# Kernel tuning notes

Hardware: AMD Instinct MI355X
Metric: run time of the kernel (lower is better)

The kernel has to match this reference:

```python
import jax, jax.numpy as jnp
import numpy as np

B, QL, DL, H = 16, 1024, 4096, 128


def setup_inputs() -> dict:
    key = jax.random.key(0)
    k1, k2, k3, k4, k5 = jax.random.split(key, 5)
    return {
        "query_input": jax.random.normal(k1, (B, QL, H), dtype=jnp.float32),
        "query_mask": jax.random.randint(k2, (B, QL), 0, 2, dtype=jnp.int32),
        "doc_input": jax.random.normal(k3, (B, DL, H), dtype=jnp.float32),
        "doc_mask": jax.random.randint(k4, (B, DL), 0, 2, dtype=jnp.int32),
        "sim_matrix": jax.random.normal(k5, (B, QL, DL), dtype=jnp.float32),
    }


def reference(query_input, query_mask, doc_input, doc_mask, sim_matrix):
    # query_input: (b, q, d); doc_input: (b, k, d); sim_matrix: (b, q, k)
    dim = query_input.shape[-1]
    scale = 1.0 / jnp.sqrt(jnp.asarray(dim, dtype=query_input.dtype))
    scores = jnp.einsum("bqd,bkd->bqk", query_input, doc_input) * scale
    # mask out padded doc positions (broadcast doc_mask over query axis)
    scores = jnp.where(doc_mask[:, None, :] == 0, jnp.asarray(-9999.0, scores.dtype), scores)
    attn = jax.nn.softmax(scores, axis=-1)  # (b, q, k)
    # sim-weighted reduction over doc axis, then sum over query axis
    query_atten_sim = jnp.sum(attn * sim_matrix, axis=-1)  # (b, q)
    return jnp.sum(query_atten_sim, axis=-1, keepdims=True)  # (b, 1)
```

## Files before the change

### kernel.cpp

```cpp
#include <hip/hip_runtime.h>
#include <hip/hip_bf16.h>

#define NB 16
#define QL 1024
#define DLEN 4096
#define HD 128

#define KCB 128
#define NKC (DLEN / KCB)
#define NIT (QL / 16)
#define SIMPAN (16 * KCB * 4)
#define QPAN (16 * HD * 4)

typedef __attribute__((ext_vector_type(8))) short short8;
typedef __attribute__((ext_vector_type(4))) float f32x4;

__device__ __forceinline__ short bf16_of(float x) {
  union { __hip_bfloat16 h; short s; } u;
  u.h = __float2bfloat16(x);
  return u.s;
}

__device__ __forceinline__ short8 cvt8(float4 a, float4 b) {
  short8 r;
  r[0] = bf16_of(a.x); r[1] = bf16_of(a.y); r[2] = bf16_of(a.z); r[3] = bf16_of(a.w);
  r[4] = bf16_of(b.x); r[5] = bf16_of(b.y); r[6] = bf16_of(b.z); r[7] = bf16_of(b.w);
  return r;
}

__global__ __launch_bounds__(256, 2) void atten_cross(
    const float* __restrict__ qin, const float* __restrict__ doc,
    const int* __restrict__ dmask, const float* __restrict__ sim,
    float2* __restrict__ ws) {
  const int flat = blockIdx.x;
  const int b = flat & 15;
  const int kc = flat >> 4;
  const int tid = threadIdx.x;
  const int w = tid >> 6;
  const int lane = tid & 63;
  const int grp = lane >> 4;
  const int li = lane & 15;
  const int k0 = kc * KCB + w * 32;

  __shared__ char simbuf[3 * SIMPAN];
  __shared__ char qbuf[3 * QPAN];

  const float* dsrc = doc + ((size_t)b * DLEN + k0 + li) * HD + grp * 8;
  short8 afr[2][4];
#pragma unroll
  for (int kt = 0; kt < 2; ++kt)
#pragma unroll
    for (int cc = 0; cc < 4; ++cc) {
      const float* p = dsrc + (size_t)kt * 16 * HD + cc * 32;
      afr[kt][cc] = cvt8(*(const float4*)p, *(const float4*)(p + 4));
    }
  const int* mp = dmask + (size_t)b * DLEN + k0 + grp * 4;
  const int4 mk0 = *(const int4*)(mp);
  const int4 mk1 = *(const int4*)(mp + 16);

  const char* gsim = (const char*)sim + ((size_t)b * QL) * (DLEN * 4) + (size_t)kc * (KCB * 4);
  const char* gq = (const char*)qin + ((size_t)b * QL) * (HD * 4);
  const char* ssrc[2];
  const char* qsrc[2];
  int sdd[2];
#pragma unroll
  for (int j = 0; j < 2; ++j) {
    const int dd = w * 2048 + j * 1024 + lane * 16;
    const int row = dd >> 9, o = dd & 511;
    const int osw = o ^ ((row & 7) << 4);
    ssrc[j] = gsim + (size_t)row * (DLEN * 4) + osw;
    qsrc[j] = gq + (size_t)row * (HD * 4) + osw;
    sdd[j] = dd;
  }

#define STAGE(it, pan)                                                         \
  {                                                                            \
    const size_t so = (size_t)(it) * (16 * DLEN * 4);                          \
    const size_t qo = (size_t)(it) * (16 * HD * 4);                            \
    _Pragma("unroll") for (int j = 0; j < 2; ++j)                              \
      __builtin_amdgcn_global_load_lds(                                        \
          (const __attribute__((address_space(1))) void*)(ssrc[j] + so),       \
          (__attribute__((address_space(3))) void*)(simbuf + (pan)*SIMPAN + sdd[j]), \
          16, 0, 0);                                                           \
    _Pragma("unroll") for (int j = 0; j < 2; ++j)                              \
      __builtin_amdgcn_global_load_lds(                                        \
          (const __attribute__((address_space(1))) void*)(qsrc[j] + qo),       \
          (__attribute__((address_space(3))) void*)(qbuf + (pan)*QPAN + sdd[j]), \
          16, 0, 0);                                                           \
  }

  constexpr float scale = 0.088388347648318447f;
  const int qxor = (li & 7) << 4;
  const int mm0[4] = {mk0.x, mk0.y, mk0.z, mk0.w};
  const int mm1[4] = {mk1.x, mk1.y, mk1.z, mk1.w};

  STAGE(0, 0);
  STAGE(1, 1);

#pragma unroll 1
  for (int it = 0; it < NIT; ++it) {
    if (it == 0)      asm volatile("s_waitcnt vmcnt(4)" ::: "memory");
    else if (it == 1) asm volatile("s_waitcnt vmcnt(5)" ::: "memory");
    else              asm volatile("s_waitcnt vmcnt(6)" ::: "memory");
    __builtin_amdgcn_s_barrier();
    asm volatile("" ::: "memory");

    {
      const int nx = (it + 2 < NIT) ? it + 2 : NIT - 1;
      STAGE(nx, (it + 2) % 3);
    }

    const char* sp = simbuf + (it % 3) * SIMPAN;
    const char* qp = qbuf + (it % 3) * QPAN;

    short8 bfrag[4];
#pragma unroll
    for (int cc = 0; cc < 4; ++cc) {
      const int o0 = grp * 32 + cc * 128;
      const float4 a = *(const float4*)(qp + li * 512 + (o0 ^ qxor));
      const float4 bb = *(const float4*)(qp + li * 512 + ((o0 + 16) ^ qxor));
      bfrag[cc] = cvt8(a, bb);
    }

    float l = 0.f, nn = 0.f;
#pragma unroll
    for (int kt = 0; kt < 2; ++kt) {
      f32x4 acc = {0.f, 0.f, 0.f, 0.f};
      acc = __builtin_amdgcn_mfma_f32_16x16x32_bf16(afr[kt][0], bfrag[0], acc, 0, 0, 0);
      acc = __builtin_amdgcn_mfma_f32_16x16x32_bf16(afr[kt][1], bfrag[1], acc, 0, 0, 0);
      acc = __builtin_amdgcn_mfma_f32_16x16x32_bf16(afr[kt][2], bfrag[2], acc, 0, 0, 0);
      acc = __builtin_amdgcn_mfma_f32_16x16x32_bf16(afr[kt][3], bfrag[3], acc, 0, 0, 0);
      const int so_ = w * 128 + kt * 64 + grp * 16;
      const f32x4 sv = *(const f32x4*)(sp + li * 512 + (so_ ^ qxor));
#pragma unroll
      for (int r = 0; r < 4; ++r) {
        float e = __expf(acc[r] * scale);
        e = (kt ? mm1[r] : mm0[r]) ? e : 0.f;
        l += e;
        nn = fmaf(e, sv[r], nn);
      }
    }

    l += __shfl_xor(l, 16, 64); l += __shfl_xor(l, 32, 64);
    nn += __shfl_xor(nn, 16, 64); nn += __shfl_xor(nn, 32, 64);
    if (lane < 16) {
      ws[((size_t)(kc * 4 + w) * NB + b) * QL + it * 16 + li] = make_float2(l, nn);
    }
  }
#undef STAGE
}

__global__ __launch_bounds__(1024) void finish(const float2* __restrict__ ws,
                                               float* __restrict__ out) {
  const int b = blockIdx.x;
  const int q = threadIdx.x;
  float l = 0.f, n = 0.f;
#pragma unroll 4
  for (int s = 0; s < NKC * 4; ++s) {
    const float2 v = ws[((size_t)s * NB + b) * QL + q];
    l += v.x;
    n += v.y;
  }
  float v = n / l;
#pragma unroll
  for (int m = 1; m <= 32; m <<= 1) v += __shfl_xor(v, m, 64);
  __shared__ float red[16];
  const int wid = threadIdx.x >> 6, lane = threadIdx.x & 63;
  if (lane == 0) red[wid] = v;
  __syncthreads();
  if (threadIdx.x < 64) {
    float t = (threadIdx.x < 16) ? red[threadIdx.x] : 0.f;
#pragma unroll
    for (int m = 1; m <= 8; m <<= 1) t += __shfl_xor(t, m, 64);
    if (threadIdx.x == 0) out[b] = t;
  }
}

extern "C" void kernel_launch(void* const* d_in, const int* in_sizes, int n_in,
                              void* d_out, int out_size, void* d_ws, size_t ws_size,
                              hipStream_t stream) {
  const float* qin = (const float*)d_in[0];
  const float* doc = (const float*)d_in[2];
  const int* dmask = (const int*)d_in[3];
  const float* sim = (const float*)d_in[4];
  float* out = (float*)d_out;
  float2* ws = (float2*)d_ws;

  dim3 grid(NB * NKC);
  atten_cross<<<grid, 256, 0, stream>>>(qin, doc, dmask, sim, ws);
  finish<<<NB, 1024, 0, stream>>>(ws, out);
}
```

Before: 111.5 us.

## Pre-convert queries to bf16 in a separate pass and double the q-tile per iteration

Adds a small pre-pass kernel that converts the fp32 query tensor to bf16 once, into workspace. The main kernel then stages half-size bf16 query panels straight into LDS, with no per-block re-conversion. It also processes 32 query rows per pipeline step instead of 16, which halves the barrier/iteration count and enlarges the sim and query LDS panels (wait counts adjusted). The cost is an extra launch plus a bf16 write and read of the queries, and higher LDS use that could reduce occupancy.

Measured after the change: 104.0 us. -6.8%, faster.

```diff
diff --git a/kernel.cpp b/kernel.cpp
--- a/kernel.cpp
+++ b/kernel.cpp
@@ -8,9 +8,10 @@
 
 #define KCB 128
 #define NKC (DLEN / KCB)
-#define NIT (QL / 16)
-#define SIMPAN (16 * KCB * 4)
-#define QPAN (16 * HD * 4)
+#define QTILE 32
+#define NIT (QL / QTILE)
+#define SIMPAN (QTILE * KCB * 4)
+#define QPAN (QTILE * HD * 2)
 
 typedef __attribute__((ext_vector_type(8))) short short8;
 typedef __attribute__((ext_vector_type(4))) float f32x4;
@@ -28,10 +29,17 @@
   return r;
 }
 
+__global__ __launch_bounds__(256) void cvt_q(const float* __restrict__ in,
+                                             short8* __restrict__ outw) {
+  const size_t i = (size_t)blockIdx.x * 256 + threadIdx.x;
+  const float* p = in + i * 8;
+  outw[i] = cvt8(*(const float4*)p, *(const float4*)(p + 4));
+}
+
 __global__ __launch_bounds__(256, 2) void atten_cross(
-    const float* __restrict__ qin, const float* __restrict__ doc,
-    const int* __restrict__ dmask, const float* __restrict__ sim,
-    float2* __restrict__ ws) {
+    const float* __restrict__ qbf_unused, const __hip_bfloat16* __restrict__ qbf,
+    const float* __restrict__ doc, const int* __restrict__ dmask,
+    const float* __restrict__ sim, float2* __restrict__ ws) {
   const int flat = blockIdx.x;
   const int b = flat & 15;
   const int kc = flat >> 4;
@@ -59,25 +67,29 @@
   const int4 mk1 = *(const int4*)(mp + 16);
 
   const char* gsim = (const char*)sim + ((size_t)b * QL) * (DLEN * 4) + (size_t)kc * (KCB * 4);
-  const char* gq = (const char*)qin + ((size_t)b * QL) * (HD * 4);
-  const char* ssrc[2];
-  const char* qsrc[2];
-  int sdd[2];
+  const char* gq = (const char*)qbf + ((size_t)b * QL) * (HD * 2);
+  const char* ssrc[4]; int sdd[4];
+#pragma unroll
+  for (int j = 0; j < 4; ++j) {
+    const int dd = (w * 4 + j) * 1024 + lane * 16;
+    const int row = dd >> 9, o = dd & 511;
+    ssrc[j] = gsim + (size_t)row * (DLEN * 4) + (o ^ ((row & 7) << 4));
+    sdd[j] = dd;
+  }
+  const char* qsrc[2]; int qdd[2];
 #pragma unroll
   for (int j = 0; j < 2; ++j) {
-    const int dd = w * 2048 + j * 1024 + lane * 16;
-    const int row = dd >> 9, o = dd & 511;
-    const int osw = o ^ ((row & 7) << 4);
-    ssrc[j] = gsim + (size_t)row * (DLEN * 4) + osw;
-    qsrc[j] = gq + (size_t)row * (HD * 4) + osw;
-    sdd[j] = dd;
+    const int dd = (w * 2 + j) * 1024 + lane * 16;
+    const int row = dd >> 8, o = dd & 255;
+    qsrc[j] = gq + (size_t)row * 256 + (o ^ ((row & 7) << 4));
+    qdd[j] = dd;
   }
 
 #define STAGE(it, pan)                                                         \
   {                                                                            \
-    const size_t so = (size_t)(it) * (16 * DLEN * 4);                          \
-    const size_t qo = (size_t)(it) * (16 * HD * 4);                            \
-    _Pragma("unroll") for (int j = 0; j < 2; ++j)                              \
+    const size_t so = (size_t)(it) * (QTILE * DLEN * 4);                       \
+    const size_t qo = (size_t)(it) * (QTILE * HD * 2);                         \
+    _Pragma("unroll") for (int j = 0; j < 4; ++j)                              \
       __builtin_amdgcn_global_load_lds(                                        \
           (const __attribute__((address_space(1))) void*)(ssrc[j] + so),       \
           (__attribute__((address_space(3))) void*)(simbuf + (pan)*SIMPAN + sdd[j]), \
@@ -85,7 +97,7 @@
     _Pragma("unroll") for (int j = 0; j < 2; ++j)                              \
       __builtin_amdgcn_global_load_lds(                                        \
           (const __attribute__((address_space(1))) void*)(qsrc[j] + qo),       \
-          (__attribute__((address_space(3))) void*)(qbuf + (pan)*QPAN + sdd[j]), \
+          (__attribute__((address_space(3))) void*)(qbuf + (pan)*QPAN + qdd[j]), \
           16, 0, 0);                                                           \
   }
 
@@ -99,9 +111,9 @@
 
 #pragma unroll 1
   for (int it = 0; it < NIT; ++it) {
-    if (it == 0)      asm volatile("s_waitcnt vmcnt(4)" ::: "memory");
-    else if (it == 1) asm volatile("s_waitcnt vmcnt(5)" ::: "memory");
-    else              asm volatile("s_waitcnt vmcnt(6)" ::: "memory");
+    if (it == 0)      asm volatile("s_waitcnt vmcnt(6)" ::: "memory");
+    else if (it == 1) asm volatile("s_waitcnt vmcnt(8)" ::: "memory");
+    else              asm volatile("s_waitcnt vmcnt(10)" ::: "memory");
     __builtin_amdgcn_s_barrier();
     asm volatile("" ::: "memory");
 
@@ -113,38 +125,36 @@
     const char* sp = simbuf + (it % 3) * SIMPAN;
     const char* qp = qbuf + (it % 3) * QPAN;
 
-    short8 bfrag[4];
-#pragma unroll
-    for (int cc = 0; cc < 4; ++cc) {
-      const int o0 = grp * 32 + cc * 128;
-      const float4 a = *(const float4*)(qp + li * 512 + (o0 ^ qxor));
-      const float4 bb = *(const float4*)(qp + li * 512 + ((o0 + 16) ^ qxor));
-      bfrag[cc] = cvt8(a, bb);
-    }
-
-    float l = 0.f, nn = 0.f;
-#pragma unroll
-    for (int kt = 0; kt < 2; ++kt) {
-      f32x4 acc = {0.f, 0.f, 0.f, 0.f};
-      acc = __builtin_amdgcn_mfma_f32_16x16x32_bf16(afr[kt][0], bfrag[0], acc, 0, 0, 0);
-      acc = __builtin_amdgcn_mfma_f32_16x16x32_bf16(afr[kt][1], bfrag[1], acc, 0, 0, 0);
-      acc = __builtin_amdgcn_mfma_f32_16x16x32_bf16(afr[kt][2], bfrag[2], acc, 0, 0, 0);
-      acc = __builtin_amdgcn_mfma_f32_16x16x32_bf16(afr[kt][3], bfrag[3], acc, 0, 0, 0);
-      const int so_ = w * 128 + kt * 64 + grp * 16;
-      const f32x4 sv = *(const f32x4*)(sp + li * 512 + (so_ ^ qxor));
-#pragma unroll
-      for (int r = 0; r < 4; ++r) {
-        float e = __expf(acc[r] * scale);
-        e = (kt ? mm1[r] : mm0[r]) ? e : 0.f;
-        l += e;
-        nn = fmaf(e, sv[r], nn);
+#pragma unroll
+    for (int s = 0; s < 2; ++s) {
+      const int row = s * 16 + li;
+      short8 bfrag[4];
+#pragma unroll
+      for (int cc = 0; cc < 4; ++cc)
+        bfrag[cc] = *(const short8*)(qp + row * 256 + ((grp * 16 + cc * 64) ^ qxor));
+
+      float l = 0.f, nn = 0.f;
+#pragma unroll
+      for (int kt = 0; kt < 2; ++kt) {
+        f32x4 acc = {0.f, 0.f, 0.f, 0.f};
+        acc = __builtin_amdgcn_mfma_f32_16x16x32_bf16(afr[kt][0], bfrag[0], acc, 0, 0, 0);
+        acc = __builtin_amdgcn_mfma_f32_16x16x32_bf16(afr[kt][1], bfrag[1], acc, 0, 0, 0);
+        acc = __builtin_amdgcn_mfma_f32_16x16x32_bf16(afr[kt][2], bfrag[2], acc, 0, 0, 0);
+        acc = __builtin_amdgcn_mfma_f32_16x16x32_bf16(afr[kt][3], bfrag[3], acc, 0, 0, 0);
+        const f32x4 sv = *(const f32x4*)(sp + row * 512 + ((w * 128 + kt * 64 + grp * 16) ^ qxor));
+#pragma unroll
+        for (int r = 0; r < 4; ++r) {
+          float e = __expf(acc[r] * scale);
+          e = (kt ? mm1[r] : mm0[r]) ? e : 0.f;
+          l += e;
+          nn = fmaf(e, sv[r], nn);
+        }
       }
-    }
-
-    l += __shfl_xor(l, 16, 64); l += __shfl_xor(l, 32, 64);
-    nn += __shfl_xor(nn, 16, 64); nn += __shfl_xor(nn, 32, 64);
-    if (lane < 16) {
-      ws[((size_t)(kc * 4 + w) * NB + b) * QL + it * 16 + li] = make_float2(l, nn);
+      l += __shfl_xor(l, 16, 64); l += __shfl_xor(l, 32, 64);
+      nn += __shfl_xor(nn, 16, 64); nn += __shfl_xor(nn, 32, 64);
+      if (lane < 16)
+        ws[((size_t)(kc * 4 + w) * NB + b) * QL + it * QTILE + s * 16 + li] =
+            make_float2(l, nn);
     }
   }
 #undef STAGE
@@ -184,9 +194,15 @@
   const int* dmask = (const int*)d_in[3];
   const float* sim = (const float*)d_in[4];
   float* out = (float*)d_out;
+
   float2* ws = (float2*)d_ws;
+  short8* qbf = (short8*)((char*)d_ws + (size_t)128 * NB * QL * 8);
+
+  const size_t q_elems = (size_t)NB * QL * HD;
+  cvt_q<<<q_elems / (8 * 256), 256, 0, stream>>>(qin, qbf);
 
   dim3 grid(NB * NKC);
-  atten_cross<<<grid, 256, 0, stream>>>(qin, doc, dmask, sim, ws);
+  atten_cross<<<grid, 256, 0, stream>>>(qin, (const __hip_bfloat16*)qbf, doc,
+                                        dmask, sim, ws);
   finish<<<NB, 1024, 0, stream>>>(ws, out);
 }
```
